# Performance work log

Measured on AMD Instinct MI355X. Metric: run time of the kernel, lower is better.

## Reference

```python
import jax, jax.numpy as jnp
import numpy as np

B, N, M = 16, 1024, 4
D = 128          # embedding_dim == nhid
VOCAB = 32000
HOPS = 3
HEADS = 4
LAYERS = 1
ALPHA = 0.2
NEG_INF = -9e15


def setup_inputs() -> dict:
    key = jax.random.key(0)
    ks = jax.random.split(key, 10)
    story = jax.random.randint(ks[0], (B, N, M), 0, VOCAB)
    kb_len = jax.random.randint(ks[1], (B,), 1, N // 2 + 1)
    conv_len = jax.random.randint(ks[2], (B,), 1, N // 2)
    hidden = jax.random.normal(ks[3], (B, D), dtype=jnp.float32)
    dh_outputs = jax.random.normal(ks[4], (B, N, D), dtype=jnp.float32)
    adj = (jax.random.uniform(ks[5], (B, N, N)) < 0.02).astype(jnp.float32)
    # learned params
    emb = 0.1 * jax.random.normal(ks[6], (HOPS + 1, VOCAB, D), dtype=jnp.float32)
    lim = 1.0 / np.sqrt(D)
    gat_W = jax.random.uniform(ks[7], (LAYERS, HOPS + 1, HEADS, D, D), minval=-lim, maxval=lim, dtype=jnp.float32)
    gat_a = jax.random.uniform(ks[8], (LAYERS, HOPS + 1, HEADS, 2 * D), minval=-lim, maxval=lim, dtype=jnp.float32)
    return {"story": story, "kb_len": kb_len, "conv_len": conv_len,
            "hidden": hidden, "dh_outputs": dh_outputs, "adj": adj,
            "emb": emb, "gat_W": gat_W, "gat_a": gat_a}


def _forward(story, kb_len, conv_len, hidden, dh_outputs, adj, emb, gat_W, gat_a):
    pos = jnp.arange(N)
    # update_pad_token_adj: self-loop for padded slots k >= (kb_len-1)+conv_len+1
    ctx = kb_len + conv_len                                  # [B]
    diag_fix = (pos[None, :] >= ctx[:, None]).astype(adj.dtype)  # [B,N]
    adj = jnp.maximum(adj, jnp.eye(N, dtype=adj.dtype)[None] * diag_fix[:, :, None])
    adj_mask = adj > 0                                       # [B,N,N]

    def add_lm(mem):
        # scatter dh_outputs[b, :conv_len[b]] into rows [kb_len[b]-1, kb_len[b]-1+conv_len[b])
        start = kb_len - 1                                   # [B]
        rel = pos[None, :] - start[:, None]                  # [B,N]
        within = (rel >= 0) & (rel < conv_len[:, None])
        gath = jnp.take_along_axis(dh_outputs, jnp.clip(rel, 0, N - 1)[:, :, None], axis=1)
        return mem + jnp.where(within[:, :, None], gath, 0.0)

    def gat_stack(x, hop_idx):
        out = x
        for l in range(LAYERS):
            W = gat_W[l, hop_idx]                            # [H,D,E]
            a = gat_a[l, hop_idx]                            # [H,2E]
            E = W.shape[-1]
            Wh = jnp.einsum('bnd,hde->hbne', out, W)         # [H,B,N,E]
            f1 = jnp.einsum('hbne,he->hbn', Wh, a[:, :E])
            f2 = jnp.einsum('hbne,he->hbn', Wh, a[:, E:])
            e = jax.nn.leaky_relu(f1[..., None] + f2[..., None, :], ALPHA)  # [H,B,N,N]
            e = jnp.where(adj_mask[None], e, NEG_INF)
            att = jax.nn.softmax(e, axis=-1)
            out = jnp.einsum('hbnm,hbme->bne', att, Wh) / HEADS  # head-mean (concat=False)
        return out

    def embed(hop_idx):
        x = jnp.sum(emb[hop_idx][story], axis=2)             # [B,N,M,D] -> [B,N,D]
        return add_lm(x)

    u = hidden
    prob_logits = None
    for hop in range(HOPS):
        A = gat_stack(embed(hop), hop)
        prob_logits = jnp.einsum('bnd,bd->bn', A, u)
        prob_soft = jax.nn.softmax(prob_logits, axis=1)
        Cm = gat_stack(embed(hop + 1), hop + 1)
        u = u + jnp.einsum('bnd,bn->bd', Cm, prob_soft)
    return jax.nn.sigmoid(prob_logits), u, prob_logits


def reference(story, kb_len, conv_len, hidden, dh_outputs, adj, emb, gat_W, gat_a):
    return _forward(story, kb_len, conv_len, hidden, dh_outputs, adj, emb, gat_W, gat_a)
```

## Files before the change

kernel.cpp:

```cpp
#include <hip/hip_runtime.h>
#include <hip/hip_bf16.h>
#include <math.h>

#define Bz 16
#define Nz 1024
#define Mz 4
#define Dz 128
#define Hz 4
#define VOCABz 32000
#define CAP 128
#define BNc (Bz * Nz)
#define NC 576

typedef __attribute__((ext_vector_type(8))) short bf16x8;
typedef __attribute__((ext_vector_type(4))) float f32x4;
typedef __attribute__((ext_vector_type(2))) _Float16 f16x2;

#if defined(__has_builtin)
#if __has_builtin(__builtin_amdgcn_fdot2)
#define FDOT2(w, s, acc) acc = __builtin_amdgcn_fdot2((w), (s), (acc), false)
#endif
#endif
#ifndef FDOT2
#define FDOT2(w, s, acc) acc += (float)(w)[0] * (float)(s)[0] + (float)(w)[1] * (float)(s)[1]
#endif

__device__ inline unsigned short rne_bf16(float x) {
    unsigned u = __float_as_uint(x);
    unsigned r = (u + 0x7FFFu + ((u >> 16) & 1u)) >> 16;
    return (unsigned short)r;
}
__device__ inline float bf16_to_f(unsigned short h) {
    return __uint_as_float(((unsigned)h) << 16);
}
__device__ inline unsigned short f32_to_f16_bits(float x) {
    _Float16 hv = (_Float16)x;
    return __builtin_bit_cast(unsigned short, hv);
}
__device__ inline unsigned pack_f16(float a, float b) {
    f16x2 p;
    p[0] = (_Float16)a;
    p[1] = (_Float16)b;
    return __builtin_bit_cast(unsigned, p);
}

__global__ __launch_bounds__(256) void k_prep(const float* __restrict__ adj,
                                              const int* __restrict__ kb_len,
                                              const int* __restrict__ conv_len,
                                              const float* __restrict__ gat_W,
                                              const float* __restrict__ gat_a,
                                              const float* __restrict__ hidden,
                                              int* __restrict__ idx, int* __restrict__ cnt,
                                              unsigned short* __restrict__ wthi,
                                              unsigned short* __restrict__ wtlo,
                                              float* __restrict__ u) {
    int blk = blockIdx.x;
    int t = threadIdx.x;
    if (blk < BNc) {
        int row = blk;
        int b = row >> 10, n = row & 1023;
        __shared__ int scnt;
        if (t == 0) scnt = 0;
        __syncthreads();
        int ctx = kb_len[b] + conv_len[b];
        const float4 av = *((const float4*)(adj + (size_t)row * Nz) + t);
        int m0 = t * 4;
#pragma unroll
        for (int k = 0; k < 4; k++) {
            float a = k == 0 ? av.x : k == 1 ? av.y : k == 2 ? av.z : av.w;
            int m = m0 + k;
            bool on = (a > 0.f) || (m == n && n >= ctx);
            if (on) {
                int p = atomicAdd(&scnt, 1);
                if (p < CAP) idx[(size_t)row * CAP + p] = m;
            }
        }
        __syncthreads();
        if (t == 0) cnt[row] = scnt < CAP ? scnt : CAP;
    } else if (blk < BNc + 1152) {
        int i = (blk - BNc) * 256 + t;
        int d = i & 127;
        int rest = i >> 7;
        int c = rest % NC;
        int hop = rest / NC;
        float v;
        if (c < 512) {
            int h = c & 3, e = c >> 2;
            v = gat_W[(((size_t)(hop * 4 + h)) * 128 + d) * 128 + e];
        } else if (c < 520) {
            int q = c - 512;
            int h = q & 3, which = q >> 2;
            const float* wrow = gat_W + (((size_t)(hop * 4 + h)) * 128 + d) * 128;
            const float* arow = gat_a + ((size_t)(hop * 4 + h)) * 256 + which * 128;
            float s = 0.f;
            for (int e = 0; e < 128; e++) s += wrow[e] * arow[e];
            v = s;
        } else {
            v = 0.f;
        }
        unsigned short h = rne_bf16(v);
        wthi[i] = h;
        wtlo[i] = rne_bf16(v - bf16_to_f(h));
    } else {
        int i = (blk - BNc - 1152) * 256 + t;
        if (i < Bz * Dz) u[i] = hidden[i];
    }
}

__global__ __launch_bounds__(128) void k_embed4(const int* __restrict__ story,
                                                const float* __restrict__ emb,
                                                const float* __restrict__ dh,
                                                const int* __restrict__ kb_len,
                                                const int* __restrict__ conv_len,
                                                unsigned short* __restrict__ xhi,
                                                unsigned short* __restrict__ xlo) {
    int row = blockIdx.x;
    int b = row >> 10, n = row & 1023;
    int d = threadIdx.x;
    const int* st = story + (size_t)row * Mz;
    int s0 = st[0], s1 = st[1], s2 = st[2], s3 = st[3];
    int rel = n - (kb_len[b] - 1);
    float dhv = (rel >= 0 && rel < conv_len[b]) ? dh[((size_t)(b << 10) + rel) * Dz + d] : 0.f;
#pragma unroll
    for (int hop = 0; hop < 4; hop++) {
        const float* ek = emb + (size_t)hop * VOCABz * Dz;
        float acc = ek[(size_t)s0 * Dz + d] + ek[(size_t)s1 * Dz + d]
                  + ek[(size_t)s2 * Dz + d] + ek[(size_t)s3 * Dz + d] + dhv;
        unsigned short hb = rne_bf16(acc);
        size_t o = (size_t)hop * BNc * Dz + (size_t)row * Dz + d;
        xhi[o] = hb;
        xlo[o] = rne_bf16(acc - bf16_to_f(hb));
    }
}

#define AST 72
__global__ __launch_bounds__(256) void k_whf4(const unsigned short* __restrict__ xhi_a,
                                              const unsigned short* __restrict__ xlo_a,
                                              const unsigned short* __restrict__ wthi_a,
                                              const unsigned short* __restrict__ wtlo_a,
                                              unsigned short* __restrict__ WhT_a,
                                              float* __restrict__ ff) {
    int blk = blockIdx.x;
    int xcd = blk & 7;
    int s = blk >> 3;
    int hop = s / 144;
    int r = s - hop * 144;
    int rt = r / 9;
    int ct = r - rt * 9;
    int row0 = (xcd * 16 + rt) * 128;
    int t = threadIdx.x;
    int wave = t >> 6, lane = t & 63;
    int quad = lane >> 4, l16 = lane & 15;

    const unsigned short* xhi = xhi_a + (size_t)hop * BNc * Dz;
    const unsigned short* xlo = xlo_a + (size_t)hop * BNc * Dz;
    const unsigned short* wthi = wthi_a + (size_t)hop * NC * 128;
    const unsigned short* wtlo = wtlo_a + (size_t)hop * NC * 128;

    __shared__ unsigned short Ah[128 * AST], Al[128 * AST];
    __shared__ unsigned short Bh[64 * AST], Bl[64 * AST];

    f32x4 acc[2][4];
#pragma unroll
    for (int mt = 0; mt < 2; mt++)
#pragma unroll
        for (int nt = 0; nt < 4; nt++) acc[mt][nt] = (f32x4)0.f;

    for (int ph = 0; ph < 2; ph++) {
        int kb = ph * 64;
        for (int i = t; i < 1024; i += 256) {
            int rr = i >> 3, c = (i & 7) * 8;
            *(uint4*)&Ah[rr * AST + c] = *(const uint4*)&xhi[(size_t)(row0 + rr) * Dz + kb + c];
            *(uint4*)&Al[rr * AST + c] = *(const uint4*)&xlo[(size_t)(row0 + rr) * Dz + kb + c];
        }
        for (int i = t; i < 512; i += 256) {
            int cr = i >> 3, cc = (i & 7) * 8;
            size_t src = ((size_t)(ct * 64 + cr)) * 128 + kb + cc;
            *(uint4*)&Bh[cr * AST + cc] = *(const uint4*)&wthi[src];
            *(uint4*)&Bl[cr * AST + cc] = *(const uint4*)&wtlo[src];
        }
        __syncthreads();
#pragma unroll
        for (int ks = 0; ks < 2; ks++) {
            int ko = ks * 32 + quad * 8;
            bf16x8 ah[2], al[2];
#pragma unroll
            for (int mt = 0; mt < 2; mt++) {
                int rr = wave * 32 + mt * 16 + l16;
                ah[mt] = *(const bf16x8*)&Ah[rr * AST + ko];
                al[mt] = *(const bf16x8*)&Al[rr * AST + ko];
            }
#pragma unroll
            for (int nt = 0; nt < 4; nt++) {
                int cc = nt * 16 + l16;
                bf16x8 bh = *(const bf16x8*)&Bh[cc * AST + ko];
                bf16x8 bl = *(const bf16x8*)&Bl[cc * AST + ko];
#pragma unroll
                for (int mt = 0; mt < 2; mt++) {
                    acc[mt][nt] = __builtin_amdgcn_mfma_f32_16x16x32_bf16(ah[mt], bh, acc[mt][nt], 0, 0, 0);
                    acc[mt][nt] = __builtin_amdgcn_mfma_f32_16x16x32_bf16(ah[mt], bl, acc[mt][nt], 0, 0, 0);
                    acc[mt][nt] = __builtin_amdgcn_mfma_f32_16x16x32_bf16(al[mt], bh, acc[mt][nt], 0, 0, 0);
                }
            }
        }
        __syncthreads();
    }

    if (ct < 8) {
        unsigned short* St = Ah;
#pragma unroll
        for (int mt = 0; mt < 2; mt++)
#pragma unroll
            for (int nt = 0; nt < 4; nt++)
#pragma unroll
                for (int reg = 0; reg < 4; reg++) {
                    int rr = wave * 32 + mt * 16 + quad * 4 + reg;
                    int cc = nt * 16 + l16;
                    St[rr * AST + cc] = f32_to_f16_bits(acc[mt][nt][reg]);
                }
        __syncthreads();
        int rr = t >> 1, seg = t & 1;
        size_t gbase = ((size_t)hop * BNc + row0 + rr) * 512 + ct * 64 + seg * 32;
#pragma unroll
        for (int k = 0; k < 4; k++) {
            uint4 vv = *(uint4*)&St[rr * AST + seg * 32 + k * 8];
            *(uint4*)&WhT_a[gbase + k * 8] = vv;
        }
    } else {
        if (l16 < 8) {
#pragma unroll
            for (int mt = 0; mt < 2; mt++)
#pragma unroll
                for (int reg = 0; reg < 4; reg++) {
                    int row = row0 + wave * 32 + mt * 16 + quad * 4 + reg;
                    ff[((size_t)hop * BNc + row) * 8 + l16] = acc[mt][0][reg];
                }
        }
    }
}

__global__ __launch_bounds__(256) void k_attn4(const unsigned short* __restrict__ WhT_a,
                                               const float* __restrict__ ff,
                                               const int* __restrict__ idx,
                                               const int* __restrict__ cnt,
                                               float* __restrict__ G_a) {
    int blk = blockIdx.x;
    int xcd = blk & 7;
    int s = blk >> 3;
    int g = s >> 8;
    int p = (g << 3) | xcd;
    int hop = p >> 4, b = p & 15;
    int wid = threadIdx.x >> 6, lane = threadIdx.x & 63;
    int n = ((s & 255) << 2) | wid;
    int row = (b << 10) | n;
    int deg = cnt[row];
    const unsigned short* WhTb = WhT_a + ((size_t)hop * BNc + ((size_t)b << 10)) * 512;
    const char* wblc = (const char*)WhTb + lane * 16;
    const float* ffh = ff + (size_t)hop * BNc * 8;
    float accx = 0.f, accy = 0.f;
    if (deg > 0) {
        int m0 = lane < deg ? idx[(size_t)row * CAP + lane] : -1;
        int m1 = lane + 64 < deg ? idx[(size_t)row * CAP + lane + 64] : -1;
        float4 f1r = *(const float4*)&ffh[(size_t)row * 8];
        int m0c = m0 < 0 ? 0 : m0, m1c = m1 < 0 ? 0 : m1;
        float4 f2a = *(const float4*)&ffh[((size_t)(b << 10) + m0c) * 8 + 4];
        float4 f2b = *(const float4*)&ffh[((size_t)(b << 10) + m1c) * 8 + 4];
        float e0[4], e1[4];
        e0[0] = f1r.x + f2a.x; e0[1] = f1r.y + f2a.y; e0[2] = f1r.z + f2a.z; e0[3] = f1r.w + f2a.w;
        e1[0] = f1r.x + f2b.x; e1[1] = f1r.y + f2b.y; e1[2] = f1r.z + f2b.z; e1[3] = f1r.w + f2b.w;
#pragma unroll
        for (int h = 0; h < 4; h++) {
            e0[h] = e0[h] >= 0.f ? e0[h] : 0.2f * e0[h];
            e1[h] = e1[h] >= 0.f ? e1[h] : 0.2f * e1[h];
            if (m0 < 0) e0[h] = -1e30f;
            if (m1 < 0) e1[h] = -1e30f;
        }
        float mx[4], sum[4];
#pragma unroll
        for (int h = 0; h < 4; h++) {
            float m = fmaxf(e0[h], e1[h]);
#pragma unroll
            for (int mm = 1; mm < 64; mm <<= 1) m = fmaxf(m, __shfl_xor(m, mm));
            mx[h] = m;
        }
        float w0[4], w1[4];
#pragma unroll
        for (int h = 0; h < 4; h++) {
            w0[h] = expf(e0[h] - mx[h]);
            w1[h] = expf(e1[h] - mx[h]);
            float sm = w0[h] + w1[h];
#pragma unroll
            for (int mm = 1; mm < 64; mm <<= 1) sm += __shfl_xor(sm, mm);
            sum[h] = sm;
        }
#pragma unroll
        for (int h = 0; h < 4; h++) {
            float inv = 0.25f / sum[h];
            w0[h] *= inv;
            w1[h] *= inv;
        }
        unsigned w01_0 = pack_f16(w0[0], w0[1]), w23_0 = pack_f16(w0[2], w0[3]);
        unsigned w01_1 = pack_f16(w1[0], w1[1]), w23_1 = pack_f16(w1[2], w1[3]);
        int moff0 = m0c << 10;
        int moff1 = m1c << 10;
        int dlo = deg < 64 ? deg : 64;
#pragma unroll 2
        for (int j = 0; j < dlo; j++) {
            int so = __builtin_amdgcn_readlane(moff0, j);
            unsigned a01 = (unsigned)__builtin_amdgcn_readlane((int)w01_0, j);
            unsigned a23 = (unsigned)__builtin_amdgcn_readlane((int)w23_0, j);
            uint4 raw = *(const uint4*)(wblc + so);
            f16x2 p01 = __builtin_bit_cast(f16x2, a01);
            f16x2 p23 = __builtin_bit_cast(f16x2, a23);
            FDOT2(__builtin_bit_cast(f16x2, raw.x), p01, accx);
            FDOT2(__builtin_bit_cast(f16x2, raw.y), p23, accx);
            FDOT2(__builtin_bit_cast(f16x2, raw.z), p01, accy);
            FDOT2(__builtin_bit_cast(f16x2, raw.w), p23, accy);
        }
        if (deg > 64) {
            for (int j = 0; j < deg - 64; j++) {
                int so = __builtin_amdgcn_readlane(moff1, j);
                unsigned a01 = (unsigned)__builtin_amdgcn_readlane((int)w01_1, j);
                unsigned a23 = (unsigned)__builtin_amdgcn_readlane((int)w23_1, j);
                uint4 raw = *(const uint4*)(wblc + so);
                f16x2 p01 = __builtin_bit_cast(f16x2, a01);
                f16x2 p23 = __builtin_bit_cast(f16x2, a23);
                FDOT2(__builtin_bit_cast(f16x2, raw.x), p01, accx);
                FDOT2(__builtin_bit_cast(f16x2, raw.y), p23, accx);
                FDOT2(__builtin_bit_cast(f16x2, raw.z), p01, accy);
                FDOT2(__builtin_bit_cast(f16x2, raw.w), p23, accy);
            }
        }
    } else {
        for (int m = 0; m < Nz; m++) {
            uint4 raw = *(const uint4*)(wblc + (m << 10));
            f16x2 a = __builtin_bit_cast(f16x2, raw.x), c = __builtin_bit_cast(f16x2, raw.y);
            f16x2 d = __builtin_bit_cast(f16x2, raw.z), e = __builtin_bit_cast(f16x2, raw.w);
            accx += (float)a[0] + (float)a[1] + (float)c[0] + (float)c[1];
            accy += (float)d[0] + (float)d[1] + (float)e[0] + (float)e[1];
        }
        accx *= 1.f / (Hz * Nz);
        accy *= 1.f / (Hz * Nz);
    }
    float2 o = make_float2(accx, accy);
    *(float2*)&G_a[((size_t)hop * BNc + row) * Dz + lane * 2] = o;
}

__global__ __launch_bounds__(256) void k_logits4(const float* __restrict__ G_a, int hopA,
                                                 const float* __restrict__ u,
                                                 float* __restrict__ logits) {
    int row = blockIdx.x * 4 + (threadIdx.x >> 6);
    int lane = threadIdx.x & 63;
    int b = row >> 10;
    const float* g = G_a + ((size_t)hopA * BNc + row) * Dz;
    const float* ub = u + b * Dz;
    float s = g[lane] * ub[lane] + g[lane + 64] * ub[lane + 64];
#pragma unroll
    for (int off = 32; off; off >>= 1) s += __shfl_down(s, off);
    if (lane == 0) logits[row] = s;
}

__global__ __launch_bounds__(256) void k_upd(const float* __restrict__ G_a, int hopC,
                                             const float* __restrict__ logits,
                                             float* __restrict__ u) {
    int b = blockIdx.x >> 3;
    int chunk = blockIdx.x & 7;
    int t = threadIdx.x;
    __shared__ float sp[1024];
    __shared__ float red[10];
    __shared__ float part[2][128];
    const float* l = logits + (size_t)b * Nz;
    float4 lv = *((const float4*)l + t);
    float mx = fmaxf(fmaxf(lv.x, lv.y), fmaxf(lv.z, lv.w));
#pragma unroll
    for (int mm = 1; mm < 64; mm <<= 1) mx = fmaxf(mx, __shfl_xor(mx, mm));
    if ((t & 63) == 0) red[t >> 6] = mx;
    __syncthreads();
    if (t == 0) {
        float m = red[0];
        for (int i = 1; i < 4; i++) m = fmaxf(m, red[i]);
        red[8] = m;
    }
    __syncthreads();
    mx = red[8];
    float e0 = expf(lv.x - mx), e1 = expf(lv.y - mx), e2 = expf(lv.z - mx), e3 = expf(lv.w - mx);
    float sum = e0 + e1 + e2 + e3;
#pragma unroll
    for (int mm = 1; mm < 64; mm <<= 1) sum += __shfl_xor(sum, mm);
    if ((t & 63) == 0) red[4 + (t >> 6)] = sum;
    __syncthreads();
    if (t == 0) {
        float ss = 0.f;
        for (int i = 0; i < 4; i++) ss += red[4 + i];
        red[9] = 1.f / ss;
    }
    __syncthreads();
    float inv = red[9];
    sp[t * 4] = e0 * inv;
    sp[t * 4 + 1] = e1 * inv;
    sp[t * 4 + 2] = e2 * inv;
    sp[t * 4 + 3] = e3 * inv;
    __syncthreads();
    int d = t & 127, half = t >> 7;
    const float* gc = G_a + ((size_t)hopC * BNc + (b << 10) + chunk * 128 + half * 64) * Dz + d;
    const float* pc = &sp[chunk * 128 + half * 64];
    float acc = 0.f;
#pragma unroll 4
    for (int j = 0; j < 64; j++) acc += gc[(size_t)j * Dz] * pc[j];
    part[half][d] = acc;
    __syncthreads();
    if (t < 128) atomicAdd(&u[b * Dz + t], part[0][t] + part[1][t]);
}

__global__ void k_fin(const float* __restrict__ logits, const float* __restrict__ u,
                      float* __restrict__ out) {
    int i = blockIdx.x * 256 + threadIdx.x;
    if (i < Bz * Nz) {
        float l = logits[i];
        out[i] = 1.f / (1.f + expf(-l));
        out[Bz * Nz + Bz * Dz + i] = l;
    }
    if (i < Bz * Dz) out[Bz * Nz + i] = u[i];
}

extern "C" void kernel_launch(void* const* d_in, const int* in_sizes, int n_in,
                              void* d_out, int out_size, void* d_ws, size_t ws_size,
                              hipStream_t stream) {
    const int*   story    = (const int*)d_in[0];
    const int*   kb_len   = (const int*)d_in[1];
    const int*   conv_len = (const int*)d_in[2];
    const float* hidden   = (const float*)d_in[3];
    const float* dh       = (const float*)d_in[4];
    const float* adj      = (const float*)d_in[5];
    const float* emb      = (const float*)d_in[6];
    const float* gat_W    = (const float*)d_in[7];
    const float* gat_a    = (const float*)d_in[8];
    float* out = (float*)d_out;

    char* w = (char*)d_ws;
    auto alloc = [&](size_t bytes) {
        char* pp = w;
        w += (bytes + 255) & ~(size_t)255;
        return pp;
    };
    const size_t BN = (size_t)Bz * Nz;
    int*            idx  = (int*)           alloc(BN * CAP * 4);
    int*            cnt  = (int*)           alloc(BN * 4);
    unsigned short* xhi  = (unsigned short*)alloc(4 * BN * Dz * 2);
    unsigned short* xlo  = (unsigned short*)alloc(4 * BN * Dz * 2);
    unsigned short* wthi = (unsigned short*)alloc(4 * NC * 128 * 2);
    unsigned short* wtlo = (unsigned short*)alloc(4 * NC * 128 * 2);
    unsigned short* WhT  = (unsigned short*)alloc(4 * BN * 512 * 2);
    float*          ff   = (float*)         alloc(4 * BN * 8 * 4);
    float*          G    = (float*)         alloc(4 * BN * Dz * 4);
    float*          logits = (float*)       alloc(BN * 4);
    float*          u    = (float*)         alloc((size_t)Bz * Dz * 4);

    k_prep<<<BNc + 1152 + 8, 256, 0, stream>>>(adj, kb_len, conv_len, gat_W, gat_a, hidden,
                                               idx, cnt, wthi, wtlo, u);
    k_embed4<<<BNc, 128, 0, stream>>>(story, emb, dh, kb_len, conv_len, xhi, xlo);
    k_whf4<<<4608, 256, 0, stream>>>(xhi, xlo, wthi, wtlo, WhT, ff);
    k_attn4<<<16384, 256, 0, stream>>>(WhT, ff, idx, cnt, G);
    for (int hop = 0; hop < 3; hop++) {
        k_logits4<<<BNc / 4, 256, 0, stream>>>(G, hop, u, logits);
        k_upd<<<Bz * 8, 256, 0, stream>>>(G, hop + 1, logits, u);
    }
    k_fin<<<(Bz * Nz + 255) / 256, 256, 0, stream>>>(logits, u, out);
}
```

Baseline: 354.5 us.

## Switch projection GEMM to fp16 split and pack two attention rows per wave

The Wh projection GEMM moves from a three-term bf16 hi/lo split (three MFMAs per tile) to an fp16 scheme. The input is split into hi/lo fp16 parts, while the weights are stored as a single fp16 array, so each tile needs two MFMAs and half the weight traffic. The attention kernel now processes two rows per wavefront, one per 32-lane half, when both degrees are at most 32. Each lane accumulates four outputs, and the grid is half the size. Rows with larger degree fall back to the previous per-row path. The fp16 weights trade some accuracy and range for fewer MFMAs and less memory traffic.

```diff
diff --git a/kernel.cpp b/kernel.cpp
--- a/kernel.cpp
+++ b/kernel.cpp
@@ -12,7 +12,8 @@
 #define BNc (Bz * Nz)
 #define NC 576
 
-typedef __attribute__((ext_vector_type(8))) short bf16x8;
+typedef __attribute__((ext_vector_type(8))) short s16x8;
+typedef __attribute__((ext_vector_type(8))) _Float16 f16x8;
 typedef __attribute__((ext_vector_type(4))) float f32x4;
 typedef __attribute__((ext_vector_type(2))) _Float16 f16x2;
 
@@ -24,18 +25,14 @@
 #ifndef FDOT2
 #define FDOT2(w, s, acc) acc += (float)(w)[0] * (float)(s)[0] + (float)(w)[1] * (float)(s)[1]
 #endif
-
-__device__ inline unsigned short rne_bf16(float x) {
-    unsigned u = __float_as_uint(x);
-    unsigned r = (u + 0x7FFFu + ((u >> 16) & 1u)) >> 16;
-    return (unsigned short)r;
-}
-__device__ inline float bf16_to_f(unsigned short h) {
-    return __uint_as_float(((unsigned)h) << 16);
-}
+#define BC16(x) __builtin_bit_cast(f16x2, (x))
+
 __device__ inline unsigned short f32_to_f16_bits(float x) {
     _Float16 hv = (_Float16)x;
     return __builtin_bit_cast(unsigned short, hv);
+}
+__device__ inline float f16_bits_to_f32(unsigned short h) {
+    return (float)__builtin_bit_cast(_Float16, h);
 }
 __device__ inline unsigned pack_f16(float a, float b) {
     f16x2 p;
@@ -51,8 +48,7 @@
                                               const float* __restrict__ gat_a,
                                               const float* __restrict__ hidden,
                                               int* __restrict__ idx, int* __restrict__ cnt,
-                                              unsigned short* __restrict__ wthi,
-                                              unsigned short* __restrict__ wtlo,
+                                              unsigned short* __restrict__ wt,
                                               float* __restrict__ u) {
     int blk = blockIdx.x;
     int t = threadIdx.x;
@@ -98,9 +94,7 @@
         } else {
             v = 0.f;
         }
-        unsigned short h = rne_bf16(v);
-        wthi[i] = h;
-        wtlo[i] = rne_bf16(v - bf16_to_f(h));
+        wt[i] = f32_to_f16_bits(v);
     } else {
         int i = (blk - BNc - 1152) * 256 + t;
         if (i < Bz * Dz) u[i] = hidden[i];
@@ -126,18 +120,17 @@
         const float* ek = emb + (size_t)hop * VOCABz * Dz;
         float acc = ek[(size_t)s0 * Dz + d] + ek[(size_t)s1 * Dz + d]
                   + ek[(size_t)s2 * Dz + d] + ek[(size_t)s3 * Dz + d] + dhv;
-        unsigned short hb = rne_bf16(acc);
+        unsigned short hb = f32_to_f16_bits(acc);
         size_t o = (size_t)hop * BNc * Dz + (size_t)row * Dz + d;
         xhi[o] = hb;
-        xlo[o] = rne_bf16(acc - bf16_to_f(hb));
+        xlo[o] = f32_to_f16_bits(acc - f16_bits_to_f32(hb));
     }
 }
 
 #define AST 72
 __global__ __launch_bounds__(256) void k_whf4(const unsigned short* __restrict__ xhi_a,
                                               const unsigned short* __restrict__ xlo_a,
-                                              const unsigned short* __restrict__ wthi_a,
-                                              const unsigned short* __restrict__ wtlo_a,
+                                              const unsigned short* __restrict__ wt_a,
                                               unsigned short* __restrict__ WhT_a,
                                               float* __restrict__ ff) {
     int blk = blockIdx.x;
@@ -154,11 +147,10 @@
 
     const unsigned short* xhi = xhi_a + (size_t)hop * BNc * Dz;
     const unsigned short* xlo = xlo_a + (size_t)hop * BNc * Dz;
-    const unsigned short* wthi = wthi_a + (size_t)hop * NC * 128;
-    const unsigned short* wtlo = wtlo_a + (size_t)hop * NC * 128;
+    const unsigned short* wt = wt_a + (size_t)hop * NC * 128;
 
     __shared__ unsigned short Ah[128 * AST], Al[128 * AST];
-    __shared__ unsigned short Bh[64 * AST], Bl[64 * AST];
+    __shared__ unsigned short Bh[64 * AST];
 
     f32x4 acc[2][4];
 #pragma unroll
@@ -175,31 +167,28 @@
         }
         for (int i = t; i < 512; i += 256) {
             int cr = i >> 3, cc = (i & 7) * 8;
-            size_t src = ((size_t)(ct * 64 + cr)) * 128 + kb + cc;
-            *(uint4*)&Bh[cr * AST + cc] = *(const uint4*)&wthi[src];
-            *(uint4*)&Bl[cr * AST + cc] = *(const uint4*)&wtlo[src];
+            *(uint4*)&Bh[cr * AST + cc] =
+                *(const uint4*)&wt[((size_t)(ct * 64 + cr)) * 128 + kb + cc];
         }
         __syncthreads();
 #pragma unroll
         for (int ks = 0; ks < 2; ks++) {
             int ko = ks * 32 + quad * 8;
-            bf16x8 ah[2], al[2];
+            f16x8 ah[2], al[2];
 #pragma unroll
             for (int mt = 0; mt < 2; mt++) {
                 int rr = wave * 32 + mt * 16 + l16;
-                ah[mt] = *(const bf16x8*)&Ah[rr * AST + ko];
-                al[mt] = *(const bf16x8*)&Al[rr * AST + ko];
+                ah[mt] = __builtin_bit_cast(f16x8, *(const s16x8*)&Ah[rr * AST + ko]);
+                al[mt] = __builtin_bit_cast(f16x8, *(const s16x8*)&Al[rr * AST + ko]);
             }
 #pragma unroll
             for (int nt = 0; nt < 4; nt++) {
                 int cc = nt * 16 + l16;
-                bf16x8 bh = *(const bf16x8*)&Bh[cc * AST + ko];
-                bf16x8 bl = *(const bf16x8*)&Bl[cc * AST + ko];
+                f16x8 bh = __builtin_bit_cast(f16x8, *(const s16x8*)&Bh[cc * AST + ko]);
 #pragma unroll
                 for (int mt = 0; mt < 2; mt++) {
-                    acc[mt][nt] = __builtin_amdgcn_mfma_f32_16x16x32_bf16(ah[mt], bh, acc[mt][nt], 0, 0, 0);
-                    acc[mt][nt] = __builtin_amdgcn_mfma_f32_16x16x32_bf16(ah[mt], bl, acc[mt][nt], 0, 0, 0);
-                    acc[mt][nt] = __builtin_amdgcn_mfma_f32_16x16x32_bf16(al[mt], bh, acc[mt][nt], 0, 0, 0);
+                    acc[mt][nt] = __builtin_amdgcn_mfma_f32_16x16x32_f16(ah[mt], bh, acc[mt][nt], 0, 0, 0);
+                    acc[mt][nt] = __builtin_amdgcn_mfma_f32_16x16x32_f16(al[mt], bh, acc[mt][nt], 0, 0, 0);
                 }
             }
         }
@@ -239,24 +228,11 @@
     }
 }
 
-__global__ __launch_bounds__(256) void k_attn4(const unsigned short* __restrict__ WhT_a,
-                                               const float* __restrict__ ff,
-                                               const int* __restrict__ idx,
-                                               const int* __restrict__ cnt,
-                                               float* __restrict__ G_a) {
-    int blk = blockIdx.x;
-    int xcd = blk & 7;
-    int s = blk >> 3;
-    int g = s >> 8;
-    int p = (g << 3) | xcd;
-    int hop = p >> 4, b = p & 15;
-    int wid = threadIdx.x >> 6, lane = threadIdx.x & 63;
-    int n = ((s & 255) << 2) | wid;
-    int row = (b << 10) | n;
-    int deg = cnt[row];
-    const unsigned short* WhTb = WhT_a + ((size_t)hop * BNc + ((size_t)b << 10)) * 512;
+__device__ void attn_row_full(const unsigned short* __restrict__ WhTb,
+                              const float* __restrict__ ffh,
+                              const int* __restrict__ idx, int deg, int b, int row,
+                              int lane, float* __restrict__ Gp) {
     const char* wblc = (const char*)WhTb + lane * 16;
-    const float* ffh = ff + (size_t)hop * BNc * 8;
     float accx = 0.f, accy = 0.f;
     if (deg > 0) {
         int m0 = lane < deg ? idx[(size_t)row * CAP + lane] : -1;
@@ -275,27 +251,18 @@
             if (m0 < 0) e0[h] = -1e30f;
             if (m1 < 0) e1[h] = -1e30f;
         }
-        float mx[4], sum[4];
+        float w0[4], w1[4];
 #pragma unroll
         for (int h = 0; h < 4; h++) {
             float m = fmaxf(e0[h], e1[h]);
 #pragma unroll
             for (int mm = 1; mm < 64; mm <<= 1) m = fmaxf(m, __shfl_xor(m, mm));
-            mx[h] = m;
-        }
-        float w0[4], w1[4];
-#pragma unroll
-        for (int h = 0; h < 4; h++) {
-            w0[h] = expf(e0[h] - mx[h]);
-            w1[h] = expf(e1[h] - mx[h]);
+            w0[h] = expf(e0[h] - m);
+            w1[h] = expf(e1[h] - m);
             float sm = w0[h] + w1[h];
 #pragma unroll
             for (int mm = 1; mm < 64; mm <<= 1) sm += __shfl_xor(sm, mm);
-            sum[h] = sm;
-        }
-#pragma unroll
-        for (int h = 0; h < 4; h++) {
-            float inv = 0.25f / sum[h];
+            float inv = 0.25f / sm;
             w0[h] *= inv;
             w1[h] *= inv;
         }
@@ -310,40 +277,114 @@
             unsigned a01 = (unsigned)__builtin_amdgcn_readlane((int)w01_0, j);
             unsigned a23 = (unsigned)__builtin_amdgcn_readlane((int)w23_0, j);
             uint4 raw = *(const uint4*)(wblc + so);
-            f16x2 p01 = __builtin_bit_cast(f16x2, a01);
-            f16x2 p23 = __builtin_bit_cast(f16x2, a23);
-            FDOT2(__builtin_bit_cast(f16x2, raw.x), p01, accx);
-            FDOT2(__builtin_bit_cast(f16x2, raw.y), p23, accx);
-            FDOT2(__builtin_bit_cast(f16x2, raw.z), p01, accy);
-            FDOT2(__builtin_bit_cast(f16x2, raw.w), p23, accy);
-        }
-        if (deg > 64) {
-            for (int j = 0; j < deg - 64; j++) {
-                int so = __builtin_amdgcn_readlane(moff1, j);
-                unsigned a01 = (unsigned)__builtin_amdgcn_readlane((int)w01_1, j);
-                unsigned a23 = (unsigned)__builtin_amdgcn_readlane((int)w23_1, j);
-                uint4 raw = *(const uint4*)(wblc + so);
-                f16x2 p01 = __builtin_bit_cast(f16x2, a01);
-                f16x2 p23 = __builtin_bit_cast(f16x2, a23);
-                FDOT2(__builtin_bit_cast(f16x2, raw.x), p01, accx);
-                FDOT2(__builtin_bit_cast(f16x2, raw.y), p23, accx);
-                FDOT2(__builtin_bit_cast(f16x2, raw.z), p01, accy);
-                FDOT2(__builtin_bit_cast(f16x2, raw.w), p23, accy);
-            }
+            f16x2 p01 = BC16(a01), p23 = BC16(a23);
+            FDOT2(BC16(raw.x), p01, accx);
+            FDOT2(BC16(raw.y), p23, accx);
+            FDOT2(BC16(raw.z), p01, accy);
+            FDOT2(BC16(raw.w), p23, accy);
+        }
+        for (int j = 0; j < deg - 64; j++) {
+            int so = __builtin_amdgcn_readlane(moff1, j);
+            unsigned a01 = (unsigned)__builtin_amdgcn_readlane((int)w01_1, j);
+            unsigned a23 = (unsigned)__builtin_amdgcn_readlane((int)w23_1, j);
+            uint4 raw = *(const uint4*)(wblc + so);
+            f16x2 p01 = BC16(a01), p23 = BC16(a23);
+            FDOT2(BC16(raw.x), p01, accx);
+            FDOT2(BC16(raw.y), p23, accx);
+            FDOT2(BC16(raw.z), p01, accy);
+            FDOT2(BC16(raw.w), p23, accy);
         }
     } else {
         for (int m = 0; m < Nz; m++) {
             uint4 raw = *(const uint4*)(wblc + (m << 10));
-            f16x2 a = __builtin_bit_cast(f16x2, raw.x), c = __builtin_bit_cast(f16x2, raw.y);
-            f16x2 d = __builtin_bit_cast(f16x2, raw.z), e = __builtin_bit_cast(f16x2, raw.w);
-            accx += (float)a[0] + (float)a[1] + (float)c[0] + (float)c[1];
-            accy += (float)d[0] + (float)d[1] + (float)e[0] + (float)e[1];
+            accx += (float)BC16(raw.x)[0] + (float)BC16(raw.x)[1]
+                  + (float)BC16(raw.y)[0] + (float)BC16(raw.y)[1];
+            accy += (float)BC16(raw.z)[0] + (float)BC16(raw.z)[1]
+                  + (float)BC16(raw.w)[0] + (float)BC16(raw.w)[1];
         }
         accx *= 1.f / (Hz * Nz);
         accy *= 1.f / (Hz * Nz);
     }
-    float2 o = make_float2(accx, accy);
-    *(float2*)&G_a[((size_t)hop * BNc + row) * Dz + lane * 2] = o;
+    *(float2*)&Gp[lane * 2] = make_float2(accx, accy);
+}
+
+__global__ __launch_bounds__(256) void k_attn4(const unsigned short* __restrict__ WhT_a,
+                                               const float* __restrict__ ff,
+                                               const int* __restrict__ idx,
+                                               const int* __restrict__ cnt,
+                                               float* __restrict__ G_a) {
+    int blk = blockIdx.x;
+    int xcd = blk & 7;
+    int s = blk >> 3;
+    int g = s >> 7;
+    int p = (g << 3) | xcd;
+    int hop = p >> 4, b = p & 15;
+    int wid = threadIdx.x >> 6, lane = threadIdx.x & 63;
+    int r2 = ((s & 127) << 2) | wid;
+    int half = lane >> 5, l32 = lane & 31;
+    int n = (r2 << 1) | half;
+    int row = (b << 10) | n;
+    const unsigned short* WhTb = WhT_a + ((size_t)hop * BNc + ((size_t)b << 10)) * 512;
+    const float* ffh = ff + (size_t)hop * BNc * 8;
+    int deg = cnt[row];
+    int deg0 = __shfl(deg, 0), deg1 = __shfl(deg, 32);
+    if (deg0 > 0 && deg1 > 0 && deg0 <= 32 && deg1 <= 32) {
+        int m = l32 < deg ? idx[(size_t)row * CAP + l32] : -1;
+        int mc = m < 0 ? 0 : m;
+        float4 f1r = *(const float4*)&ffh[(size_t)row * 8];
+        float4 f2m = *(const float4*)&ffh[((size_t)(b << 10) + mc) * 8 + 4];
+        float e[4];
+        e[0] = f1r.x + f2m.x; e[1] = f1r.y + f2m.y; e[2] = f1r.z + f2m.z; e[3] = f1r.w + f2m.w;
+        float w[4];
+#pragma unroll
+        for (int h = 0; h < 4; h++) {
+            e[h] = e[h] >= 0.f ? e[h] : 0.2f * e[h];
+            if (m < 0) e[h] = -1e30f;
+        }
+#pragma unroll
+        for (int h = 0; h < 4; h++) {
+            float mx = e[h];
+#pragma unroll
+            for (int mm = 1; mm < 32; mm <<= 1) mx = fmaxf(mx, __shfl_xor(mx, mm));
+            w[h] = expf(e[h] - mx);
+            float sm = w[h];
+#pragma unroll
+            for (int mm = 1; mm < 32; mm <<= 1) sm += __shfl_xor(sm, mm);
+            w[h] *= 0.25f / sm;
+        }
+        int w01 = (int)pack_f16(w[0], w[1]);
+        int w23 = (int)pack_f16(w[2], w[3]);
+        int moff = mc << 10;
+        int dmax = deg0 > deg1 ? deg0 : deg1;
+        int srcbase = lane & 32;
+        const char* wbl = (const char*)WhTb + l32 * 32;
+        float a0 = 0.f, a1 = 0.f, a2 = 0.f, a3 = 0.f;
+#pragma unroll 2
+        for (int j = 0; j < dmax; j++) {
+            int src = srcbase + j;
+            int vo = __shfl(moff, src);
+            unsigned b01 = (unsigned)__shfl(w01, src);
+            unsigned b23 = (unsigned)__shfl(w23, src);
+            uint4 r0 = *(const uint4*)(wbl + vo);
+            uint4 r1 = *(const uint4*)(wbl + vo + 16);
+            f16x2 p01 = BC16(b01), p23 = BC16(b23);
+            FDOT2(BC16(r0.x), p01, a0);
+            FDOT2(BC16(r0.y), p23, a0);
+            FDOT2(BC16(r0.z), p01, a1);
+            FDOT2(BC16(r0.w), p23, a1);
+            FDOT2(BC16(r1.x), p01, a2);
+            FDOT2(BC16(r1.y), p23, a2);
+            FDOT2(BC16(r1.z), p01, a3);
+            FDOT2(BC16(r1.w), p23, a3);
+        }
+        *(float4*)&G_a[((size_t)hop * BNc + row) * Dz + l32 * 4] = make_float4(a0, a1, a2, a3);
+    } else {
+        int row0 = (b << 10) | (r2 << 1);
+        attn_row_full(WhTb, ffh, idx, deg0, b, row0, lane,
+                      &G_a[((size_t)hop * BNc + row0) * Dz]);
+        attn_row_full(WhTb, ffh, idx, deg1, b, row0 + 1, lane,
+                      &G_a[((size_t)hop * BNc + row0 + 1) * Dz]);
+    }
 }
 
 __global__ __launch_bounds__(256) void k_logits4(const float* __restrict__ G_a, int hopA,
@@ -448,8 +489,7 @@
     int*            cnt  = (int*)           alloc(BN * 4);
     unsigned short* xhi  = (unsigned short*)alloc(4 * BN * Dz * 2);
     unsigned short* xlo  = (unsigned short*)alloc(4 * BN * Dz * 2);
-    unsigned short* wthi = (unsigned short*)alloc(4 * NC * 128 * 2);
-    unsigned short* wtlo = (unsigned short*)alloc(4 * NC * 128 * 2);
+    unsigned short* wt   = (unsigned short*)alloc(4 * NC * 128 * 2);
     unsigned short* WhT  = (unsigned short*)alloc(4 * BN * 512 * 2);
     float*          ff   = (float*)         alloc(4 * BN * 8 * 4);
     float*          G    = (float*)         alloc(4 * BN * Dz * 4);
@@ -457,10 +497,10 @@
     float*          u    = (float*)         alloc((size_t)Bz * Dz * 4);
 
     k_prep<<<BNc + 1152 + 8, 256, 0, stream>>>(adj, kb_len, conv_len, gat_W, gat_a, hidden,
-                                               idx, cnt, wthi, wtlo, u);
+                                               idx, cnt, wt, u);
     k_embed4<<<BNc, 128, 0, stream>>>(story, emb, dh, kb_len, conv_len, xhi, xlo);
-    k_whf4<<<4608, 256, 0, stream>>>(xhi, xlo, wthi, wtlo, WhT, ff);
-    k_attn4<<<16384, 256, 0, stream>>>(WhT, ff, idx, cnt, G);
+    k_whf4<<<4608, 256, 0, stream>>>(xhi, xlo, wt, WhT, ff);
+    k_attn4<<<8192, 256, 0, stream>>>(WhT, ff, idx, cnt, G);
     for (int hop = 0; hop < 3; hop++) {
         k_logits4<<<BNc / 4, 256, 0, stream>>>(G, hop, u, logits);
         k_upd<<<Bz * 8, 256, 0, stream>>>(G, hop + 1, logits, u);
```

Result: faster. 329.4 us (-7.1%).
